# Kernel tuning notes

Hardware: AMD Instinct MI355X
Metric: run time of the kernel (lower is better)

Reference implementation:

```python
import jax, jax.numpy as jnp
import numpy as np
import math

B, M, C = 256, 256, 1024
ALPHA = 0.1

def setup_inputs() -> dict:
    key = jax.random.key(0)
    k1, k2 = jax.random.split(key)
    input_encoded = jax.random.normal(k1, (B, C), dtype=jnp.float32)
    memory_mean = jax.random.normal(k2, (M, C), dtype=jnp.float32)
    return {"input_encoded": input_encoded, "memory_mean": memory_mean}

def reference(input_encoded, memory_mean):
    b, c = input_encoded.shape
    m = memory_mean.shape[0]
    # ---- write_to_memory ----
    # similarity of each input with each prior memory slot: [B, M]
    sims = jnp.einsum('bc,mc->bm', input_encoded, memory_mean)
    closest_idx = jnp.argmax(sims, axis=1)                      # [B]
    sel = memory_mean[closest_idx]                              # [B, C]
    new_row = (1.0 - ALPHA) * sel + ALPHA * input_encoded       # [B, C]
    onehot = (jnp.arange(m)[None, :] == closest_idx[:, None])   # [B, M] bool
    mem = jnp.broadcast_to(memory_mean[None], (b, m, c))
    updated_memory = jnp.where(onehot[:, :, None], new_row[:, None, :], mem)  # [B, M, C]
    dkl_write = 0.5 * jnp.sum((input_encoded - sel) ** 2, axis=1)             # [B]
    # ---- read_with_encoded_input ----
    scale = 1.0 / math.sqrt(c)
    scores = jnp.einsum('bc,bmc->bm', input_encoded, updated_memory) * scale  # [B, M]
    attn = jax.nn.softmax(scores, axis=1)
    z_read = jnp.einsum('bm,bmc->bc', attn, updated_memory)                   # [B, C]
    dkl_read = 0.5 * jnp.sum((z_read - input_encoded) ** 2, axis=1)           # [B]
    kl_div = dkl_write + dkl_read
    return z_read, updated_memory, kl_div
```

## Files before the change

kernel.cpp:

```cpp
#include <hip/hip_runtime.h>
#include <math.h>

#define B_DIM 256
#define M_DIM 256
#define C_DIM 1024
#define C4    256
#define UM_OFF (B_DIM * C_DIM)
#define KL_OFF (UM_OFF + B_DIM * M_DIM * C_DIM)
#define SCALE  0.03125f

__device__ __forceinline__ float dot4(float4 a, float4 b) {
    return a.x*b.x + a.y*b.y + a.z*b.z + a.w*b.w;
}
__device__ __forceinline__ float wsum(float v) {
    #pragma unroll
    for (int off = 32; off; off >>= 1) v += __shfl_xor(v, off, 64);
    return v;
}
__device__ __forceinline__ float wmax(float v) {
    #pragma unroll
    for (int off = 32; off; off >>= 1) v = fmaxf(v, __shfl_xor(v, off, 64));
    return v;
}
__device__ __forceinline__ float4 blend9(float4 v, float4 xr) {
    return make_float4(0.9f*v.x + 0.1f*xr.x, 0.9f*v.y + 0.1f*xr.y,
                       0.9f*v.z + 0.1f*xr.z, 0.9f*v.w + 0.1f*xr.w);
}

__global__ __launch_bounds__(256) void tm_main(const float* __restrict__ x,
                                               const float* __restrict__ mem,
                                               float* __restrict__ out,
                                               int* __restrict__ idx_ws) {
    const int bid = blockIdx.x;
    const int t = threadIdx.x;
    const float4* mem4 = (const float4*)mem;

    if (bid >= B_DIM) {
        const int j  = bid - B_DIM;
        const int b  = j >> 5;
        const int m0 = (j & 31) << 3;
        const float4* src = mem4 + (m0 << 8) + t;
        float4 r0 = src[0 << 8];
        float4 r1 = src[1 << 8];
        float4 r2 = src[2 << 8];
        float4 r3 = src[3 << 8];
        float4 r4 = src[4 << 8];
        float4 r5 = src[5 << 8];
        float4 r6 = src[6 << 8];
        float4 r7 = src[7 << 8];
        float4* dst = (float4*)(out + UM_OFF) + ((size_t)b << 16) + (m0 << 8) + t;
        dst[0 << 8] = r0;
        dst[1 << 8] = r1;
        dst[2 << 8] = r2;
        dst[3 << 8] = r3;
        dst[4 << 8] = r4;
        dst[5 << 8] = r5;
        dst[6 << 8] = r6;
        dst[7 << 8] = r7;
        return;
    }

    const int b = bid;
    const int lane = t & 63;
    const int wv = t >> 6;

    __shared__ float4 s_x[C4];
    __shared__ float  s_sims[M_DIM];
    __shared__ float  s_attn[M_DIM];
    __shared__ float  s_w0[4], s_w1[4];

    float4 xv = ((const float4*)(x + (size_t)b * C_DIM))[t];
    s_x[t] = xv;
    __syncthreads();

    const float4 xr0 = s_x[lane];
    const float4 xr1 = s_x[lane + 64];
    const float4 xr2 = s_x[lane + 128];
    const float4 xr3 = s_x[lane + 192];
    #pragma unroll 4
    for (int i = 0; i < 64; ++i) {
        const int m = (wv << 6) | i;
        const float4* mr = mem4 + (m << 8);
        float acc = dot4(mr[lane],     xr0) + dot4(mr[lane+64],  xr1)
                  + dot4(mr[lane+128], xr2) + dot4(mr[lane+192], xr3);
        acc = wsum(acc);
        if (lane == 0) s_sims[m] = acc;
    }
    __syncthreads();

    const float v0 = s_sims[lane];
    const float v1 = s_sims[lane + 64];
    const float v2 = s_sims[lane + 128];
    const float v3 = s_sims[lane + 192];
    const float n2 = wsum(dot4(xr0,xr0) + dot4(xr1,xr1) + dot4(xr2,xr2) + dot4(xr3,xr3));

    float av = v0; int am = lane;
    if (v1 > av) { av = v1; am = lane + 64; }
    if (v2 > av) { av = v2; am = lane + 128; }
    if (v3 > av) { av = v3; am = lane + 192; }
    #pragma unroll
    for (int off = 32; off; off >>= 1) {
        float ov = __shfl_xor(av, off, 64);
        int   oi = __shfl_xor(am, off, 64);
        if (ov > av || (ov == av && oi < am)) { av = ov; am = oi; }
    }
    const int idx = am;
    if (t == 0) idx_ws[b] = idx;
    const float fused = 0.9f * av + 0.1f * n2;

    float s0 = ((lane      ) == idx ? fused : v0) * SCALE;
    float s1 = ((lane +  64) == idx ? fused : v1) * SCALE;
    float s2 = ((lane + 128) == idx ? fused : v2) * SCALE;
    float s3 = ((lane + 192) == idx ? fused : v3) * SCALE;
    const float mx = wmax(fmaxf(fmaxf(s0, s1), fmaxf(s2, s3)));
    const float e0 = expf(s0 - mx), e1 = expf(s1 - mx);
    const float e2 = expf(s2 - mx), e3 = expf(s3 - mx);
    const float inv = 1.0f / wsum(e0 + e1 + e2 + e3);
    const float a0 = e0 * inv, a1 = e1 * inv, a2 = e2 * inv, a3 = e3 * inv;

    if (wv == 0) {
        s_attn[lane]       = a0;
        s_attn[lane + 64]  = a1;
        s_attn[lane + 128] = a2;
        s_attn[lane + 192] = a3;
    }

    float aidx;
    if      (idx <  64) aidx = __shfl(a0, idx,       64);
    else if (idx < 128) aidx = __shfl(a1, idx - 64,  64);
    else if (idx < 192) aidx = __shfl(a2, idx - 128, 64);
    else                aidx = __shfl(a3, idx - 192, 64);
    aidx *= 0.1f;
    __syncthreads();

    float4 z = make_float4(0.f, 0.f, 0.f, 0.f);
    #pragma unroll 8
    for (int m = 0; m < M_DIM; ++m) {
        const float a = s_attn[m];
        float4 v = mem4[(m << 8) + t];
        z.x = fmaf(a, v.x, z.x);
        z.y = fmaf(a, v.y, z.y);
        z.z = fmaf(a, v.z, z.z);
        z.w = fmaf(a, v.w, z.w);
    }
    float4 sl = mem4[(idx << 8) + t];
    float4 d = make_float4(xv.x - sl.x, xv.y - sl.y, xv.z - sl.z, xv.w - sl.w);
    const float dwp = dot4(d, d);
    z.x = fmaf(aidx, d.x, z.x);
    z.y = fmaf(aidx, d.y, z.y);
    z.z = fmaf(aidx, d.z, z.z);
    z.w = fmaf(aidx, d.w, z.w);
    float ex = z.x - xv.x, ey = z.y - xv.y, ez = z.z - xv.z, ew = z.w - xv.w;
    const float drp = ex*ex + ey*ey + ez*ez + ew*ew;
    ((float4*)out)[(size_t)b * C4 + t] = z;

    const float sw = wsum(dwp);
    const float sr = wsum(drp);
    if (lane == 0) { s_w0[wv] = sw; s_w1[wv] = sr; }
    __syncthreads();
    if (t == 0)
        out[KL_OFF + b] = 0.5f * (s_w0[0]+s_w0[1]+s_w0[2]+s_w0[3]
                                + s_w1[0]+s_w1[1]+s_w1[2]+s_w1[3]);
}

__global__ __launch_bounds__(256) void tm_fix(const float* __restrict__ x,
                                              const float* __restrict__ mem,
                                              const int* __restrict__ idx_ws,
                                              float* __restrict__ out_um) {
    const int b = blockIdx.x;
    const int t = threadIdx.x;
    const int idx = idx_ws[b];
    float4 sl = ((const float4*)mem)[(idx << 8) + t];
    float4 xv = ((const float4*)(x + (size_t)b * C_DIM))[t];
    ((float4*)out_um)[((size_t)b << 16) + (idx << 8) + t] = blend9(sl, xv);
}

extern "C" void kernel_launch(void* const* d_in, const int* in_sizes, int n_in,
                              void* d_out, int out_size, void* d_ws, size_t ws_size,
                              hipStream_t stream) {
    const float* x   = (const float*)d_in[0];
    const float* mem = (const float*)d_in[1];
    float* out = (float*)d_out;
    int* idx_ws = (int*)d_ws;

    tm_main<<<dim3(B_DIM + 8192), dim3(256), 0, stream>>>(x, mem, out, idx_ws);
    tm_fix<<<dim3(B_DIM), dim3(256), 0, stream>>>(x, mem, idx_ws, out + UM_OFF);
}
```

Before: 69.49 us.

## Process four batch rows per compute block and four copies per streaming block

Compute blocks now handle four batch rows at once, so each memory row loaded for the similarity and read-out passes is reused across four inputs, with attention weights stored transposed for float4 access. The broadcast-copy blocks each load an 8-row memory slab once and write it to four batch slices, cutting the block count and the redundant loads. The grid drops from 8448 to 2112 blocks. Register pressure rises from holding sixteen x float4s and four accumulators, and only 64 compute blocks leave fewer waves for the latency-bound phase.

```diff
diff --git a/kernel.cpp b/kernel.cpp
--- a/kernel.cpp
+++ b/kernel.cpp
@@ -8,6 +8,8 @@
 #define UM_OFF (B_DIM * C_DIM)
 #define KL_OFF (UM_OFF + B_DIM * M_DIM * C_DIM)
 #define SCALE  0.03125f
+#define NPRE   64
+#define NSTRM  2048
 
 __device__ __forceinline__ float dot4(float4 a, float4 b) {
     return a.x*b.x + a.y*b.y + a.z*b.z + a.w*b.w;
@@ -35,9 +37,9 @@
     const int t = threadIdx.x;
     const float4* mem4 = (const float4*)mem;
 
-    if (bid >= B_DIM) {
-        const int j  = bid - B_DIM;
-        const int b  = j >> 5;
+    if (bid >= NPRE) {
+        const int j  = bid - NPRE;
+        const int b0 = (j >> 5) << 2;
         const int m0 = (j & 31) << 3;
         const float4* src = mem4 + (m0 << 8) + t;
         float4 r0 = src[0 << 8];
@@ -48,119 +50,191 @@
         float4 r5 = src[5 << 8];
         float4 r6 = src[6 << 8];
         float4 r7 = src[7 << 8];
-        float4* dst = (float4*)(out + UM_OFF) + ((size_t)b << 16) + (m0 << 8) + t;
-        dst[0 << 8] = r0;
-        dst[1 << 8] = r1;
-        dst[2 << 8] = r2;
-        dst[3 << 8] = r3;
-        dst[4 << 8] = r4;
-        dst[5 << 8] = r5;
-        dst[6 << 8] = r6;
-        dst[7 << 8] = r7;
+        float4* dstb = (float4*)(out + UM_OFF);
+        #pragma unroll
+        for (int jb = 0; jb < 4; ++jb) {
+            float4* dst = dstb + ((size_t)(b0 + jb) << 16) + (m0 << 8) + t;
+            dst[0 << 8] = r0;
+            dst[1 << 8] = r1;
+            dst[2 << 8] = r2;
+            dst[3 << 8] = r3;
+            dst[4 << 8] = r4;
+            dst[5 << 8] = r5;
+            dst[6 << 8] = r6;
+            dst[7 << 8] = r7;
+        }
         return;
     }
 
-    const int b = bid;
     const int lane = t & 63;
     const int wv = t >> 6;
-
-    __shared__ float4 s_x[C4];
-    __shared__ float  s_sims[M_DIM];
-    __shared__ float  s_attn[M_DIM];
-    __shared__ float  s_w0[4], s_w1[4];
-
-    float4 xv = ((const float4*)(x + (size_t)b * C_DIM))[t];
-    s_x[t] = xv;
-    __syncthreads();
-
-    const float4 xr0 = s_x[lane];
-    const float4 xr1 = s_x[lane + 64];
-    const float4 xr2 = s_x[lane + 128];
-    const float4 xr3 = s_x[lane + 192];
-    #pragma unroll 4
-    for (int i = 0; i < 64; ++i) {
-        const int m = (wv << 6) | i;
-        const float4* mr = mem4 + (m << 8);
-        float acc = dot4(mr[lane],     xr0) + dot4(mr[lane+64],  xr1)
-                  + dot4(mr[lane+128], xr2) + dot4(mr[lane+192], xr3);
-        acc = wsum(acc);
-        if (lane == 0) s_sims[m] = acc;
-    }
-    __syncthreads();
-
-    const float v0 = s_sims[lane];
-    const float v1 = s_sims[lane + 64];
-    const float v2 = s_sims[lane + 128];
-    const float v3 = s_sims[lane + 192];
-    const float n2 = wsum(dot4(xr0,xr0) + dot4(xr1,xr1) + dot4(xr2,xr2) + dot4(xr3,xr3));
-
-    float av = v0; int am = lane;
-    if (v1 > av) { av = v1; am = lane + 64; }
-    if (v2 > av) { av = v2; am = lane + 128; }
-    if (v3 > av) { av = v3; am = lane + 192; }
+    const int b0 = bid << 2;
+
+    __shared__ float4 s_x[4][C4];
+    __shared__ float  s_sims[4][M_DIM];
+    __shared__ float  s_attnT[M_DIM*4];
+    __shared__ float  s_aidx[4];
+    __shared__ float  s_dw[4];
+    __shared__ int    s_idxv[4];
+    __shared__ float4 s_red4[4];
+
     #pragma unroll
-    for (int off = 32; off; off >>= 1) {
-        float ov = __shfl_xor(av, off, 64);
-        int   oi = __shfl_xor(am, off, 64);
-        if (ov > av || (ov == av && oi < am)) { av = ov; am = oi; }
-    }
-    const int idx = am;
-    if (t == 0) idx_ws[b] = idx;
-    const float fused = 0.9f * av + 0.1f * n2;
-
-    float s0 = ((lane      ) == idx ? fused : v0) * SCALE;
-    float s1 = ((lane +  64) == idx ? fused : v1) * SCALE;
-    float s2 = ((lane + 128) == idx ? fused : v2) * SCALE;
-    float s3 = ((lane + 192) == idx ? fused : v3) * SCALE;
-    const float mx = wmax(fmaxf(fmaxf(s0, s1), fmaxf(s2, s3)));
-    const float e0 = expf(s0 - mx), e1 = expf(s1 - mx);
-    const float e2 = expf(s2 - mx), e3 = expf(s3 - mx);
-    const float inv = 1.0f / wsum(e0 + e1 + e2 + e3);
-    const float a0 = e0 * inv, a1 = e1 * inv, a2 = e2 * inv, a3 = e3 * inv;
-
-    if (wv == 0) {
-        s_attn[lane]       = a0;
-        s_attn[lane + 64]  = a1;
-        s_attn[lane + 128] = a2;
-        s_attn[lane + 192] = a3;
-    }
-
-    float aidx;
-    if      (idx <  64) aidx = __shfl(a0, idx,       64);
-    else if (idx < 128) aidx = __shfl(a1, idx - 64,  64);
-    else if (idx < 192) aidx = __shfl(a2, idx - 128, 64);
-    else                aidx = __shfl(a3, idx - 192, 64);
-    aidx *= 0.1f;
-    __syncthreads();
-
-    float4 z = make_float4(0.f, 0.f, 0.f, 0.f);
+    for (int j = 0; j < 4; ++j)
+        s_x[j][t] = ((const float4*)(x + (size_t)(b0 + j) * C_DIM))[t];
+    __syncthreads();
+
+    {
+        const float4 x00 = s_x[0][lane], x01 = s_x[0][lane+64], x02 = s_x[0][lane+128], x03 = s_x[0][lane+192];
+        const float4 x10 = s_x[1][lane], x11 = s_x[1][lane+64], x12 = s_x[1][lane+128], x13 = s_x[1][lane+192];
+        const float4 x20 = s_x[2][lane], x21 = s_x[2][lane+64], x22 = s_x[2][lane+128], x23 = s_x[2][lane+192];
+        const float4 x30 = s_x[3][lane], x31 = s_x[3][lane+64], x32 = s_x[3][lane+128], x33 = s_x[3][lane+192];
+        #pragma unroll 2
+        for (int i = 0; i < 64; ++i) {
+            const int m = (wv << 6) | i;
+            const float4* mr = mem4 + (m << 8);
+            float4 a0 = mr[lane];
+            float4 a1 = mr[lane + 64];
+            float4 a2 = mr[lane + 128];
+            float4 a3 = mr[lane + 192];
+            float p0 = dot4(a0,x00) + dot4(a1,x01) + dot4(a2,x02) + dot4(a3,x03);
+            float p1 = dot4(a0,x10) + dot4(a1,x11) + dot4(a2,x12) + dot4(a3,x13);
+            float p2 = dot4(a0,x20) + dot4(a1,x21) + dot4(a2,x22) + dot4(a3,x23);
+            float p3 = dot4(a0,x30) + dot4(a1,x31) + dot4(a2,x32) + dot4(a3,x33);
+            #pragma unroll
+            for (int off = 32; off; off >>= 1) {
+                p0 += __shfl_xor(p0, off, 64);
+                p1 += __shfl_xor(p1, off, 64);
+                p2 += __shfl_xor(p2, off, 64);
+                p3 += __shfl_xor(p3, off, 64);
+            }
+            if (lane == 0) {
+                s_sims[0][m] = p0; s_sims[1][m] = p1;
+                s_sims[2][m] = p2; s_sims[3][m] = p3;
+            }
+        }
+    }
+    __syncthreads();
+
+    {
+        const int j = wv;
+        const float v0 = s_sims[j][lane];
+        const float v1 = s_sims[j][lane + 64];
+        const float v2 = s_sims[j][lane + 128];
+        const float v3 = s_sims[j][lane + 192];
+        const float4 xa = s_x[j][lane], xb = s_x[j][lane + 64];
+        const float4 xc = s_x[j][lane + 128], xd = s_x[j][lane + 192];
+        const float n2 = wsum(dot4(xa,xa) + dot4(xb,xb) + dot4(xc,xc) + dot4(xd,xd));
+
+        float av = v0; int am = lane;
+        if (v1 > av) { av = v1; am = lane + 64; }
+        if (v2 > av) { av = v2; am = lane + 128; }
+        if (v3 > av) { av = v3; am = lane + 192; }
+        #pragma unroll
+        for (int off = 32; off; off >>= 1) {
+            float ov = __shfl_xor(av, off, 64);
+            int   oi = __shfl_xor(am, off, 64);
+            if (ov > av || (ov == av && oi < am)) { av = ov; am = oi; }
+        }
+        const int idx = am;
+        const float fused = 0.9f * av + 0.1f * n2;
+
+        float s0 = ((lane      ) == idx ? fused : v0) * SCALE;
+        float s1 = ((lane +  64) == idx ? fused : v1) * SCALE;
+        float s2 = ((lane + 128) == idx ? fused : v2) * SCALE;
+        float s3 = ((lane + 192) == idx ? fused : v3) * SCALE;
+        const float mx = wmax(fmaxf(fmaxf(s0, s1), fmaxf(s2, s3)));
+        const float e0 = expf(s0 - mx), e1 = expf(s1 - mx);
+        const float e2 = expf(s2 - mx), e3 = expf(s3 - mx);
+        const float inv = 1.0f / wsum(e0 + e1 + e2 + e3);
+        const float a0 = e0 * inv, a1 = e1 * inv, a2 = e2 * inv, a3 = e3 * inv;
+
+        s_attnT[(lane      ) * 4 + j] = a0;
+        s_attnT[(lane +  64) * 4 + j] = a1;
+        s_attnT[(lane + 128) * 4 + j] = a2;
+        s_attnT[(lane + 192) * 4 + j] = a3;
+
+        float aidx;
+        if      (idx <  64) aidx = __shfl(a0, idx,       64);
+        else if (idx < 128) aidx = __shfl(a1, idx - 64,  64);
+        else if (idx < 192) aidx = __shfl(a2, idx - 128, 64);
+        else                aidx = __shfl(a3, idx - 192, 64);
+
+        const float4* ir = mem4 + (idx << 8);
+        float4 q0 = ir[lane], q1 = ir[lane+64], q2 = ir[lane+128], q3 = ir[lane+192];
+        float p = 0.f; float4 dq;
+        dq = make_float4(xa.x-q0.x, xa.y-q0.y, xa.z-q0.z, xa.w-q0.w); p += dot4(dq,dq);
+        dq = make_float4(xb.x-q1.x, xb.y-q1.y, xb.z-q1.z, xb.w-q1.w); p += dot4(dq,dq);
+        dq = make_float4(xc.x-q2.x, xc.y-q2.y, xc.z-q2.z, xc.w-q2.w); p += dot4(dq,dq);
+        dq = make_float4(xd.x-q3.x, xd.y-q3.y, xd.z-q3.z, xd.w-q3.w); p += dot4(dq,dq);
+        const float dwv = wsum(p);
+
+        if (lane == 0) {
+            s_idxv[j] = idx;
+            s_aidx[j] = aidx * 0.1f;
+            s_dw[j]   = dwv;
+            idx_ws[b0 + j] = idx;
+        }
+    }
+    __syncthreads();
+
+    float4 z0 = make_float4(0,0,0,0), z1 = z0, z2 = z0, z3 = z0;
+    const float4* attn4 = (const float4*)s_attnT;
     #pragma unroll 8
     for (int m = 0; m < M_DIM; ++m) {
-        const float a = s_attn[m];
         float4 v = mem4[(m << 8) + t];
-        z.x = fmaf(a, v.x, z.x);
-        z.y = fmaf(a, v.y, z.y);
-        z.z = fmaf(a, v.z, z.z);
-        z.w = fmaf(a, v.w, z.w);
-    }
-    float4 sl = mem4[(idx << 8) + t];
-    float4 d = make_float4(xv.x - sl.x, xv.y - sl.y, xv.z - sl.z, xv.w - sl.w);
-    const float dwp = dot4(d, d);
-    z.x = fmaf(aidx, d.x, z.x);
-    z.y = fmaf(aidx, d.y, z.y);
-    z.z = fmaf(aidx, d.z, z.z);
-    z.w = fmaf(aidx, d.w, z.w);
-    float ex = z.x - xv.x, ey = z.y - xv.y, ez = z.z - xv.z, ew = z.w - xv.w;
-    const float drp = ex*ex + ey*ey + ez*ez + ew*ew;
-    ((float4*)out)[(size_t)b * C4 + t] = z;
-
-    const float sw = wsum(dwp);
-    const float sr = wsum(drp);
-    if (lane == 0) { s_w0[wv] = sw; s_w1[wv] = sr; }
-    __syncthreads();
-    if (t == 0)
-        out[KL_OFF + b] = 0.5f * (s_w0[0]+s_w0[1]+s_w0[2]+s_w0[3]
-                                + s_w1[0]+s_w1[1]+s_w1[2]+s_w1[3]);
+        float4 a = attn4[m];
+        z0.x = fmaf(a.x, v.x, z0.x); z0.y = fmaf(a.x, v.y, z0.y);
+        z0.z = fmaf(a.x, v.z, z0.z); z0.w = fmaf(a.x, v.w, z0.w);
+        z1.x = fmaf(a.y, v.x, z1.x); z1.y = fmaf(a.y, v.y, z1.y);
+        z1.z = fmaf(a.y, v.z, z1.z); z1.w = fmaf(a.y, v.w, z1.w);
+        z2.x = fmaf(a.z, v.x, z2.x); z2.y = fmaf(a.z, v.y, z2.y);
+        z2.z = fmaf(a.z, v.z, z2.z); z2.w = fmaf(a.z, v.w, z2.w);
+        z3.x = fmaf(a.w, v.x, z3.x); z3.y = fmaf(a.w, v.y, z3.y);
+        z3.z = fmaf(a.w, v.z, z3.z); z3.w = fmaf(a.w, v.w, z3.w);
+    }
+
+    float4 dr4;
+    {
+        float drp[4];
+        float4 zz[4] = { z0, z1, z2, z3 };
+        #pragma unroll
+        for (int j = 0; j < 4; ++j) {
+            const int idxj = s_idxv[j];
+            const float aj = s_aidx[j];
+            float4 sl = mem4[(idxj << 8) + t];
+            float4 xj = s_x[j][t];
+            float4 d = make_float4(xj.x - sl.x, xj.y - sl.y, xj.z - sl.z, xj.w - sl.w);
+            zz[j].x = fmaf(aj, d.x, zz[j].x);
+            zz[j].y = fmaf(aj, d.y, zz[j].y);
+            zz[j].z = fmaf(aj, d.z, zz[j].z);
+            zz[j].w = fmaf(aj, d.w, zz[j].w);
+            float ex = zz[j].x - xj.x, ey = zz[j].y - xj.y;
+            float ez = zz[j].z - xj.z, ew = zz[j].w - xj.w;
+            drp[j] = ex*ex + ey*ey + ez*ez + ew*ew;
+            ((float4*)out)[(size_t)(b0 + j) * C4 + t] = zz[j];
+        }
+        dr4 = make_float4(drp[0], drp[1], drp[2], drp[3]);
+        #pragma unroll
+        for (int off = 32; off; off >>= 1) {
+            dr4.x += __shfl_xor(dr4.x, off, 64);
+            dr4.y += __shfl_xor(dr4.y, off, 64);
+            dr4.z += __shfl_xor(dr4.z, off, 64);
+            dr4.w += __shfl_xor(dr4.w, off, 64);
+        }
+    }
+    if (lane == 0) s_red4[wv] = dr4;
+    __syncthreads();
+    if (t == 0) {
+        float4 s = s_red4[0];
+        s.x += s_red4[1].x + s_red4[2].x + s_red4[3].x;
+        s.y += s_red4[1].y + s_red4[2].y + s_red4[3].y;
+        s.z += s_red4[1].z + s_red4[2].z + s_red4[3].z;
+        s.w += s_red4[1].w + s_red4[2].w + s_red4[3].w;
+        out[KL_OFF + b0 + 0] = 0.5f * (s_dw[0] + s.x);
+        out[KL_OFF + b0 + 1] = 0.5f * (s_dw[1] + s.y);
+        out[KL_OFF + b0 + 2] = 0.5f * (s_dw[2] + s.z);
+        out[KL_OFF + b0 + 3] = 0.5f * (s_dw[3] + s.w);
+    }
 }
 
 __global__ __launch_bounds__(256) void tm_fix(const float* __restrict__ x,
@@ -183,6 +257,6 @@
     float* out = (float*)d_out;
     int* idx_ws = (int*)d_ws;
 
-    tm_main<<<dim3(B_DIM + 8192), dim3(256), 0, stream>>>(x, mem, out, idx_ws);
+    tm_main<<<dim3(NPRE + NSTRM), dim3(256), 0, stream>>>(x, mem, out, idx_ws);
     tm_fix<<<dim3(B_DIM), dim3(256), 0, stream>>>(x, mem, idx_ws, out + UM_OFF);
 }
```

Measured after the change: 84.18 us. 21.1% more time.
